# Kernel optimization log

Hardware: AMD Instinct MI355X
Metric: run time of the kernel (lower is better)

Reference implementation:

```python
import jax, jax.numpy as jnp
import numpy as np

EMBED = 384
HEADS = 12
DH = EMBED // HEADS  # 32, lucidrains default dim_heads = dim // heads
EPS = 1e-5


def _layernorm(t, g, b):
    mu = jnp.mean(t, axis=-1, keepdims=True)
    var = jnp.mean(jnp.square(t - mu), axis=-1, keepdims=True)
    return (t - mu) * jax.lax.rsqrt(var + EPS) * g + b


def _self_attn(t2, Wq, Wkv, Wo, bo):
    # t2: (N, T, D) -> multi-head self attention (lucidrains SelfAttention)
    N, T, D = t2.shape
    q = t2 @ Wq
    k, v = jnp.split(t2 @ Wkv, 2, axis=-1)
    def split_heads(z):
        return z.reshape(N, T, HEADS, DH).transpose(0, 2, 1, 3)  # (N,H,T,DH)
    q, k, v = map(split_heads, (q, k, v))
    dots = jnp.einsum('nhie,nhje->nhij', q, k) * (DH ** -0.5)
    o = jnp.einsum('nhij,nhje->nhie', jax.nn.softmax(dots, axis=-1), v)
    o = o.transpose(0, 2, 1, 3).reshape(N, T, D)
    return o @ Wo + bo


def _axial(xcl, axis, Wq, Wkv, Wo, bo):
    # xcl channels-last: (b, 3, 16, 16, C); attend along `axis` (1, 2 or 3)
    y = jnp.moveaxis(xcl, axis, -2)
    sh = y.shape
    o = _self_attn(y.reshape(-1, sh[-2], sh[-1]), Wq, Wkv, Wo, bo)
    return jnp.moveaxis(o.reshape(sh), -2, axis)


def setup_inputs() -> dict:
    key = jax.random.key(0)
    ks = jax.random.split(key, 24)
    d, mlp = EMBED, 4 * EMBED
    s = 0.02
    inp = {'x': jax.random.normal(ks[0], (128, 384, 3, 16, 16), jnp.float32)}
    for i in range(3):  # one SelfAttention per axial dim (slice, h, w)
        inp[f'Wq{i}'] = (jax.random.normal(ks[1 + 3 * i], (d, d)) * s).astype(jnp.float32)
        inp[f'Wkv{i}'] = (jax.random.normal(ks[2 + 3 * i], (d, 2 * d)) * s).astype(jnp.float32)
        inp[f'Wo{i}'] = (jax.random.normal(ks[3 + 3 * i], (d, d)) * s).astype(jnp.float32)
        inp[f'bo{i}'] = jnp.zeros((d,), jnp.float32)
    inp['g1'] = jnp.ones((d,), jnp.float32)
    inp['be1'] = jnp.zeros((d,), jnp.float32)
    inp['W1m'] = (jax.random.normal(ks[10], (d, mlp)) * s).astype(jnp.float32)
    inp['b1m'] = jnp.zeros((mlp,), jnp.float32)
    inp['W2m'] = (jax.random.normal(ks[11], (mlp, d)) * s).astype(jnp.float32)
    inp['b2m'] = jnp.zeros((d,), jnp.float32)
    inp['g2'] = jnp.ones((d,), jnp.float32)
    inp['be2'] = jnp.zeros((d,), jnp.float32)
    return inp


def reference(x, Wq0, Wkv0, Wo0, bo0, Wq1, Wkv1, Wo1, bo1, Wq2, Wkv2, Wo2, bo2,
              g1, be1, W1m, b1m, W2m, b2m, g2, be2):
    # x: (B, C=384, 3, 16, 16); dropout is identity in eval mode
    xcl = jnp.moveaxis(x, 1, -1)  # (B, 3, 16, 16, C)
    attn = (_axial(xcl, 1, Wq0, Wkv0, Wo0, bo0)
            + _axial(xcl, 2, Wq1, Wkv1, Wo1, bo1)
            + _axial(xcl, 3, Wq2, Wkv2, Wo2, bo2))  # sum_axial_out=True
    xcl = xcl + attn  # residual
    B = xcl.shape[0]
    t = xcl.reshape(B, 3 * 16 * 16, EMBED)  # == x.flatten(2).transpose(1,2)
    t = _layernorm(t, g1, be1)
    m = jax.nn.gelu(t @ W1m + b1m, approximate=False) @ W2m + b2m
    t = _layernorm(t + m, g2, be2)
    return jnp.moveaxis(t.reshape(B, 3, 16, 16, EMBED), -1, 1)
```

## Files before the change

### kernel.cpp

```cpp
#include <hip/hip_runtime.h>

typedef unsigned short u16;
typedef __bf16 bf16;
typedef bf16  bf16x4 __attribute__((ext_vector_type(4)));
typedef bf16  bf16x8 __attribute__((ext_vector_type(8)));
typedef float f32x4  __attribute__((ext_vector_type(4)));

__device__ __forceinline__ u16  f2b(float v) { return __builtin_bit_cast(u16, (bf16)v); }
__device__ __forceinline__ float b2f(u16 b)  { return (float)__builtin_bit_cast(bf16, b); }

__global__ void probe_dtype(const float* xf, int* flag) {
    __shared__ int cnt[256];
    const int tid = threadIdx.x;
    int good = 0;
#pragma unroll
    for (int i = 0; i < 4; ++i) {
        const float a = fabsf(xf[tid * 4 + i]);
        if (a > 9.5e-7f && a < 1.0e6f) good++;
    }
    cnt[tid] = good;
    __syncthreads();
    if (tid == 0) { int s = 0; for (int i = 0; i < 256; ++i) s += cnt[i]; *flag = (s > 512) ? 1 : 0; }
}

__global__ void cvt_vec(const void* in, bf16* out, int n, const int* flag) {
    const int f32 = *flag;
    for (int i = blockIdx.x * 256 + threadIdx.x; i < n; i += gridDim.x * 256)
        out[i] = f32 ? (bf16)(((const float*)in)[i])
                     : __builtin_bit_cast(bf16, ((const u16*)in)[i]);
}

__global__ void transpose_cvt(const void* in, u16* out, size_t base_off, int R, int C, const int* flag) {
    __shared__ u16 tile[32][34];
    const int f32 = *flag;
    const int c0 = blockIdx.x * 32, r0 = blockIdx.y * 32;
    const size_t bi = base_off + (size_t)blockIdx.z * R * C;
    const size_t bo = (size_t)blockIdx.z * R * C;
    const int tx = threadIdx.x, ty = threadIdx.y;
#pragma unroll
    for (int i = 0; i < 4; ++i) {
        const size_t idx = bi + (size_t)(r0 + ty + i * 8) * C + c0 + tx;
        tile[ty + i * 8][tx] = f32 ? f2b(((const float*)in)[idx]) : ((const u16*)in)[idx];
    }
    __syncthreads();
#pragma unroll
    for (int i = 0; i < 4; ++i)
        out[bo + (size_t)(c0 + ty + i * 8) * R + r0 + tx] = tile[tx][ty + i * 8];
}

__global__ void transpose_out(const u16* in, void* out, size_t base_off, int R, int C, const int* flag) {
    __shared__ u16 tile[32][34];
    const int f32 = *flag;
    const int c0 = blockIdx.x * 32, r0 = blockIdx.y * 32;
    const size_t bi = (size_t)blockIdx.z * R * C;
    const size_t bo = base_off + (size_t)blockIdx.z * R * C;
    const int tx = threadIdx.x, ty = threadIdx.y;
#pragma unroll
    for (int i = 0; i < 4; ++i)
        tile[ty + i * 8][tx] = in[bi + (size_t)(r0 + ty + i * 8) * C + c0 + tx];
    __syncthreads();
#pragma unroll
    for (int i = 0; i < 4; ++i) {
        const size_t o = bo + (size_t)(c0 + ty + i * 8) * R + r0 + tx;
        const u16 v = tile[tx][ty + i * 8];
        if (f32) ((float*)out)[o] = b2f(v); else ((u16*)out)[o] = v;
    }
}

__device__ __forceinline__ void gld_lds16(const bf16* g, bf16* l) {
    __builtin_amdgcn_global_load_lds((__attribute__((address_space(1))) void*)g,
                                     (__attribute__((address_space(3))) void*)l,
                                     16, 0, 0);
}

template<int MODE>
__global__ __launch_bounds__(256)
void gemm_bt(const bf16* __restrict__ A, const bf16* __restrict__ BT,
             bf16* C, const bf16* __restrict__ bias,
             const bf16* add, int M, int N, int K)
{
    __shared__ __align__(16) bf16 sm[4][8192];
    const int tid = threadIdx.x;

    const int gx = gridDim.x, gy = gridDim.y;
    int lin = blockIdx.y * gx + blockIdx.x;
    const int nwg = gx * gy;
    const int q = nwg >> 3, r8 = nwg & 7;
    const int xcd = lin & 7, idx = lin >> 3;
    lin = (xcd < r8 ? xcd * (q + 1) : r8 * (q + 1) + (xcd - r8) * q) + idx;
    const int bm0 = (lin / gy) * 128;
    const int bn0 = (lin % gy) * 128;

    const int lane = tid & 63, wid = tid >> 6;
    const int wr = wid >> 1, wc = wid & 1;
    const int fr = lane & 15, fg = lane >> 4;
    const int arow = tid >> 3;
    const int scol = ((tid & 7) ^ (arow & 7)) << 3;

    const bf16* Ab = A  + (size_t)(bm0 + arow) * K + scol;
    const bf16* Bb = BT + (size_t)(bn0 + arow) * K + scol;

    f32x4 acc[4][4] = {};

    const int NT = K >> 6;
    {
        bf16* la = sm[0];
        bf16* lb = sm[1];
#pragma unroll
        for (int i = 0; i < 4; ++i) gld_lds16(Ab + (size_t)i * 32 * K, &la[i * 2048 + tid * 8]);
#pragma unroll
        for (int i = 0; i < 4; ++i) gld_lds16(Bb + (size_t)i * 32 * K, &lb[i * 2048 + tid * 8]);
    }
    __syncthreads();

    const int sw = fr & 7;
    for (int t = 0; t < NT; ++t) {
        if (t + 1 < NT) {
            const int k0 = (t + 1) << 6;
            bf16* la = sm[2 * ((t + 1) & 1)];
            bf16* lb = sm[2 * ((t + 1) & 1) + 1];
#pragma unroll
            for (int i = 0; i < 4; ++i) gld_lds16(Ab + k0 + (size_t)i * 32 * K, &la[i * 2048 + tid * 8]);
#pragma unroll
            for (int i = 0; i < 4; ++i) gld_lds16(Bb + k0 + (size_t)i * 32 * K, &lb[i * 2048 + tid * 8]);
        }
        const bf16* la = sm[2 * (t & 1)];
        const bf16* lb = sm[2 * (t & 1) + 1];
#pragma unroll
        for (int kk = 0; kk < 2; ++kk) {
            bf16x8 af[4], bfv[4];
#pragma unroll
            for (int m = 0; m < 4; ++m) {
                const int rr = wr * 64 + m * 16 + fr;
                af[m] = *(const bf16x8*)&la[rr * 64 + ((((kk << 2) + fg) ^ sw) << 3)];
            }
#pragma unroll
            for (int n = 0; n < 4; ++n) {
                const int rr = wc * 64 + n * 16 + fr;
                bfv[n] = *(const bf16x8*)&lb[rr * 64 + ((((kk << 2) + fg) ^ sw) << 3)];
            }
#pragma unroll
            for (int m = 0; m < 4; ++m)
#pragma unroll
                for (int n = 0; n < 4; ++n)
                    acc[m][n] = __builtin_amdgcn_mfma_f32_16x16x32_bf16(af[m], bfv[n], acc[m][n], 0, 0, 0);
        }
        __syncthreads();
    }

    float* lc = (float*)sm;
#pragma unroll
    for (int n = 0; n < 4; ++n) {
        const int col = wc * 64 + n * 16 + fr;
#pragma unroll
        for (int m = 0; m < 4; ++m) {
            const int row0 = wr * 64 + m * 16 + fg * 4;
#pragma unroll
            for (int r2 = 0; r2 < 4; ++r2)
                lc[(row0 + r2) * 128 + col] = acc[m][n][r2];
        }
    }
    __syncthreads();
    const f32x4* lc4 = (const f32x4*)sm;
#pragma unroll
    for (int i = 0; i < 16; ++i) {
        const int chunk = i * 256 + tid;
        const int row = chunk >> 5, cb = (chunk & 31) * 4;
        const size_t goff = (size_t)(bm0 + row) * N + bn0 + cb;
        const f32x4 v = lc4[chunk];
        bf16x4 o;
        if (MODE == 0) {
#pragma unroll
            for (int e = 0; e < 4; ++e) o[e] = (bf16)v[e];
        } else if (MODE == 1) {
            const bf16x4 bv = *(const bf16x4*)&bias[bn0 + cb];
            const bf16x4 av = *(const bf16x4*)&add[goff];
#pragma unroll
            for (int e = 0; e < 4; ++e) o[e] = (bf16)(v[e] + (float)bv[e] + (float)av[e]);
        } else {
            const bf16x4 bv = *(const bf16x4*)&bias[bn0 + cb];
#pragma unroll
            for (int e = 0; e < 4; ++e) {
                const float x = v[e] + (float)bv[e];
                o[e] = (bf16)(0.5f * x * (1.f + erff(x * 0.70710678118654752f)));
            }
        }
        *(bf16x4*)&C[goff] = o;
    }
}

__global__ __launch_bounds__(256)
void attn16(const bf16* __restrict__ QKV, bf16* __restrict__ O, int tstride, int lastmul)
{
    const int lane = threadIdx.x & 63;
    const int gw   = (blockIdx.x * 256 + threadIdx.x) >> 6;
    const int head = gw % 12;
    const int seq  = gw / 12;
    const int b    = seq / 48, r2 = seq % 48;
    const int s    = r2 >> 4, last = r2 & 15;
    const int tbase = b * 768 + s * 256 + last * lastmul;
    const int fr = lane & 15, fg = lane >> 4;

    const size_t rowQ = (size_t)(tbase + fr * tstride) * 1152 + head * 32 + fg * 8;
    const bf16x8 kf = *(const bf16x8*)(QKV + rowQ + 384);
    const bf16x8 qf = *(const bf16x8*)(QKV + rowQ);
    const f32x4 z = {0.f, 0.f, 0.f, 0.f};
    f32x4 S = __builtin_amdgcn_mfma_f32_16x16x32_bf16(kf, qf, z, 0, 0, 0);

    const float sc = 0.17677669529663687f;
    float mx = fmaxf(fmaxf(S[0], S[1]), fmaxf(S[2], S[3]));
    mx = fmaxf(mx, __shfl_xor(mx, 16));
    mx = fmaxf(mx, __shfl_xor(mx, 32));
    float p[4], sum = 0.f;
#pragma unroll
    for (int r = 0; r < 4; ++r) { p[r] = __expf((S[r] - mx) * sc); sum += p[r]; }
    sum += __shfl_xor(sum, 16);
    sum += __shfl_xor(sum, 32);
    const float inv = 1.f / sum;

    bf16x8 pa;
#pragma unroll
    for (int j = 0; j < 8; ++j) {
        const int srcg = 2 * fg + (j >> 2);
        const float v = __shfl(p[j & 3], fr + 16 * (srcg & 3));
        pa[j] = (bf16)(fg < 2 ? v * inv : 0.f);
    }

#pragma unroll
    for (int t = 0; t < 2; ++t) {
        bf16x8 vf;
#pragma unroll
        for (int j = 0; j < 8; ++j) {
            const int key = fg * 8 + j;
            vf[j] = (fg < 2)
                ? QKV[(size_t)(tbase + key * tstride) * 1152 + 768 + head * 32 + fr + 16 * t]
                : (bf16)0.f;
        }
        f32x4 o = __builtin_amdgcn_mfma_f32_16x16x32_bf16(pa, vf, z, 0, 0, 0);
#pragma unroll
        for (int r = 0; r < 4; ++r)
            O[(size_t)(tbase + (fg * 4 + r) * tstride) * 384 + head * 32 + fr + 16 * t] = (bf16)o[r];
    }
}

__global__ __launch_bounds__(256)
void attn3(const bf16* __restrict__ QKV, bf16* __restrict__ O)
{
    const int t    = blockIdx.x * 256 + threadIdx.x;
    const int head = t % 12;
    const int seq  = t / 12;
    const int b    = seq >> 8, hw = seq & 255;
    const size_t base  = (size_t)(b * 768 + hw) * 1152 + head * 32;
    const size_t tstep = (size_t)256 * 1152;

    float s[3][3] = {};
#pragma unroll
    for (int c = 0; c < 4; ++c) {
        bf16x8 q[3], k[3];
#pragma unroll
        for (int i = 0; i < 3; ++i) {
            q[i] = *(const bf16x8*)(QKV + base + i * tstep + c * 8);
            k[i] = *(const bf16x8*)(QKV + base + i * tstep + 384 + c * 8);
        }
#pragma unroll
        for (int i = 0; i < 3; ++i)
#pragma unroll
            for (int j = 0; j < 3; ++j) {
                float a = 0.f;
#pragma unroll
                for (int e = 0; e < 8; ++e) a += (float)q[i][e] * (float)k[j][e];
                s[i][j] += a;
            }
    }
    const float sc = 0.17677669529663687f;
    float p[3][3];
#pragma unroll
    for (int i = 0; i < 3; ++i) {
        const float mx = fmaxf(s[i][0], fmaxf(s[i][1], s[i][2]));
        float sum = 0.f;
#pragma unroll
        for (int j = 0; j < 3; ++j) { p[i][j] = __expf((s[i][j] - mx) * sc); sum += p[i][j]; }
        const float inv = 1.f / sum;
#pragma unroll
        for (int j = 0; j < 3; ++j) p[i][j] *= inv;
    }
    const size_t obase = (size_t)(b * 768 + hw) * 384 + head * 32;
#pragma unroll
    for (int c = 0; c < 4; ++c) {
        bf16x8 v[3];
#pragma unroll
        for (int j = 0; j < 3; ++j) v[j] = *(const bf16x8*)(QKV + base + j * tstep + 768 + c * 8);
#pragma unroll
        for (int i = 0; i < 3; ++i) {
            bf16x8 ov;
#pragma unroll
            for (int e = 0; e < 8; ++e)
                ov[e] = (bf16)(p[i][0] * (float)v[0][e] + p[i][1] * (float)v[1][e] + p[i][2] * (float)v[2][e]);
            *(bf16x8*)(O + obase + (size_t)i * 256 * 384 + c * 8) = ov;
        }
    }
}

__global__ __launch_bounds__(256)
void ln_kernel(const bf16* __restrict__ in, bf16* __restrict__ out,
               const bf16* __restrict__ g, const bf16* __restrict__ be, int ntok)
{
    const int w    = (blockIdx.x * 256 + threadIdx.x) >> 6;
    const int lane = threadIdx.x & 63;
    if (w >= ntok) return;
    const bf16* row = in + (size_t)w * 384;
    float x[6], sum = 0.f;
#pragma unroll
    for (int i = 0; i < 6; ++i) { x[i] = (float)row[lane + i * 64]; sum += x[i]; }
#pragma unroll
    for (int o = 32; o >= 1; o >>= 1) sum += __shfl_xor(sum, o);
    const float mu = sum * (1.f / 384.f);
    float vs = 0.f;
#pragma unroll
    for (int i = 0; i < 6; ++i) { const float d = x[i] - mu; vs += d * d; }
#pragma unroll
    for (int o = 32; o >= 1; o >>= 1) vs += __shfl_xor(vs, o);
    const float rstd = rsqrtf(vs * (1.f / 384.f) + 1e-5f);
    bf16* orow = out + (size_t)w * 384;
#pragma unroll
    for (int i = 0; i < 6; ++i)
        orow[lane + i * 64] = (bf16)((x[i] - mu) * rstd * (float)g[lane + i * 64] + (float)be[lane + i * 64]);
}

extern "C" void kernel_launch(void* const* d_in, const int* in_sizes, int n_in,
                              void* d_out, int out_size, void* d_ws, size_t ws_size,
                              hipStream_t stream)
{
    const void* x = d_in[0];
    const void *Wq[3], *Wkv[3], *Wo[3], *bo[3];
    for (int i = 0; i < 3; ++i) {
        Wq[i]  = d_in[1 + 4 * i];
        Wkv[i] = d_in[2 + 4 * i];
        Wo[i]  = d_in[3 + 4 * i];
        bo[i]  = d_in[4 + 4 * i];
    }
    const void* g1  = d_in[13];
    const void* be1 = d_in[14];
    const void* W1m = d_in[15];
    const void* b1m = d_in[16];
    const void* W2m = d_in[17];
    const void* b2m = d_in[18];
    const void* g2  = d_in[19];
    const void* be2 = d_in[20];

    char* ws = (char*)d_ws;
    const size_t WB = 6ull * 1024 * 1024;
    bf16* wqkvT[3]; bf16* woT[3];
    for (int i = 0; i < 3; ++i) {
        wqkvT[i] = (bf16*)(ws + (size_t)i * 884736ull);
        woT[i]   = (bf16*)(ws + 2654208ull + (size_t)i * 294912ull);
    }
    bf16* w1mT = (bf16*)(ws + 3538944ull);
    bf16* w2mT = (bf16*)(ws + 4718592ull);
    bf16* vbo[3]; bf16 *vg1, *vbe1, *vg2, *vbe2, *vb1m, *vb2m;
    {
        char* vp = ws + 5898240ull;
        vbo[0] = (bf16*)(vp);            vbo[1] = (bf16*)(vp + 768);  vbo[2] = (bf16*)(vp + 1536);
        vg1  = (bf16*)(vp + 2304);       vbe1 = (bf16*)(vp + 3072);
        vg2  = (bf16*)(vp + 3840);       vbe2 = (bf16*)(vp + 4608);
        vb1m = (bf16*)(vp + 5376);       vb2m = (bf16*)(vp + 8448);
    }
    int* dflag = (int*)(ws + 5908480ull);

    int NB = 32;
    while (NB > 1) {
        size_t need = WB + (size_t)NB * 768 * (4 * 384 + 1536) * 2;
        if (need <= ws_size) break;
        NB >>= 1;
    }
    const int Tc = NB * 768;
    const size_t tokB = (size_t)Tc * 384 * 2;
    bf16* Xc   = (bf16*)(ws + WB);
    bf16* ABc  = (bf16*)(ws + WB + tokB);
    bf16* T1c  = (bf16*)(ws + WB + 2 * tokB);
    bf16* ATOc = (bf16*)(ws + WB + 3 * tokB);
    bf16* BIGc = (bf16*)(ws + WB + 4 * tokB);

    probe_dtype<<<1, 256, 0, stream>>>((const float*)x, dflag);
    for (int i = 0; i < 3; ++i)
        cvt_vec<<<2, 256, 0, stream>>>(bo[i], vbo[i], 384, dflag);
    cvt_vec<<<2, 256, 0, stream>>>(g1,  vg1,  384,  dflag);
    cvt_vec<<<2, 256, 0, stream>>>(be1, vbe1, 384,  dflag);
    cvt_vec<<<2, 256, 0, stream>>>(g2,  vg2,  384,  dflag);
    cvt_vec<<<2, 256, 0, stream>>>(be2, vbe2, 384,  dflag);
    cvt_vec<<<6, 256, 0, stream>>>(b1m, vb1m, 1536, dflag);
    cvt_vec<<<2, 256, 0, stream>>>(b2m, vb2m, 384,  dflag);

    const dim3 tb(32, 8);
    for (int i = 0; i < 3; ++i) {
        transpose_cvt<<<dim3(12, 12, 1), tb, 0, stream>>>(Wq[i],  (u16*)wqkvT[i],               0, 384, 384, dflag);
        transpose_cvt<<<dim3(24, 12, 1), tb, 0, stream>>>(Wkv[i], (u16*)(wqkvT[i] + 384 * 384), 0, 384, 768, dflag);
        transpose_cvt<<<dim3(12, 12, 1), tb, 0, stream>>>(Wo[i],  (u16*)woT[i],                 0, 384, 384, dflag);
    }
    transpose_cvt<<<dim3(48, 12, 1), tb, 0, stream>>>(W1m, (u16*)w1mT, 0, 384, 1536, dflag);
    transpose_cvt<<<dim3(12, 48, 1), tb, 0, stream>>>(W2m, (u16*)w2mT, 0, 1536, 384, dflag);

    for (int b0 = 0; b0 < 128; b0 += NB) {
        const size_t xoff = (size_t)b0 * 384 * 768;
        transpose_cvt<<<dim3(24, 12, NB), tb, 0, stream>>>(x, (u16*)Xc, xoff, 384, 768, dflag);

        for (int i = 0; i < 3; ++i) {
            gemm_bt<0><<<dim3(Tc / 128, 9), 256, 0, stream>>>(Xc, wqkvT[i], BIGc, nullptr, nullptr, Tc, 1152, 384);
            if (i == 0)      attn3 <<<NB * 12,  256, 0, stream>>>(BIGc, ATOc);
            else if (i == 1) attn16<<<NB * 144, 256, 0, stream>>>(BIGc, ATOc, 16, 1);
            else             attn16<<<NB * 144, 256, 0, stream>>>(BIGc, ATOc, 1, 16);
            gemm_bt<1><<<dim3(Tc / 128, 3), 256, 0, stream>>>(ATOc, woT[i], ABc, vbo[i], (i == 0) ? Xc : ABc, Tc, 384, 384);
        }
        ln_kernel<<<Tc / 4, 256, 0, stream>>>(ABc, T1c, vg1, vbe1, Tc);
        gemm_bt<2><<<dim3(Tc / 128, 12), 256, 0, stream>>>(T1c, w1mT, BIGc, vb1m, nullptr, Tc, 1536, 384);
        gemm_bt<1><<<dim3(Tc / 128, 3),  256, 0, stream>>>(BIGc, w2mT, ABc, vb2m, T1c, Tc, 384, 1536);
        ln_kernel<<<Tc / 4, 256, 0, stream>>>(ABc, Xc, vg2, vbe2, Tc);
        transpose_out<<<dim3(12, 24, NB), tb, 0, stream>>>((const u16*)Xc, d_out, xoff, 768, 384, dflag);
    }
}
```

Measured before the change: 1.559 ms.

## Fuse three axial QKV projections into one 256-tile GEMM, add 256-tile MLP up GEMM

Concatenates the three per-axis QKV weight matrices into one 3584-row weight, zero-padded from 3456 rows. A new 256x256-tile, 512-thread GEMM computes all Q/K/V projections in a single launch, and the attention kernels read from it with a wider row stride. The same larger-tile kernel also replaces the MLP up-projection with fused GELU, and it writes bf16 through LDS with vector stores. The intent is fewer launches, more reuse of the A tile, and better MFMA efficiency. The cost is a larger intermediate buffer, which can lower the chunk size NB, plus 128 padded rows of wasted compute and 128 KB of LDS per block.

```diff
diff --git a/kernel.cpp b/kernel.cpp
--- a/kernel.cpp
+++ b/kernel.cpp
@@ -28,6 +28,10 @@
     for (int i = blockIdx.x * 256 + threadIdx.x; i < n; i += gridDim.x * 256)
         out[i] = f32 ? (bf16)(((const float*)in)[i])
                      : __builtin_bit_cast(bf16, ((const u16*)in)[i]);
+}
+
+__global__ void zfill(bf16* p, int n) {
+    for (int i = blockIdx.x * 256 + threadIdx.x; i < n; i += gridDim.x * 256) p[i] = (bf16)0.f;
 }
 
 __global__ void transpose_cvt(const void* in, u16* out, size_t base_off, int R, int C, const int* flag) {
@@ -71,6 +75,101 @@
     __builtin_amdgcn_global_load_lds((__attribute__((address_space(1))) void*)g,
                                      (__attribute__((address_space(3))) void*)l,
                                      16, 0, 0);
+}
+
+template<int MODE>
+__global__ __launch_bounds__(512)
+void gemm256(const bf16* __restrict__ A, const bf16* __restrict__ BT,
+             bf16* C, const bf16* __restrict__ bias, int M, int N, int K)
+{
+    __shared__ __align__(16) bf16 sm[65536];
+    const int tid = threadIdx.x;
+
+    const int gx = gridDim.x, gy = gridDim.y;
+    int lin = blockIdx.y * gx + blockIdx.x;
+    const int nwg = gx * gy;
+    const int q = nwg >> 3, r8 = nwg & 7;
+    const int xcd = lin & 7, idx = lin >> 3;
+    lin = (xcd < r8 ? xcd * (q + 1) : r8 * (q + 1) + (xcd - r8) * q) + idx;
+    const int bm0 = (lin / gy) * 256;
+    const int bn0 = (lin % gy) * 256;
+
+    const int lane = tid & 63, wid = tid >> 6;
+    const int wr = wid >> 2, wc = wid & 3;
+    const int fr = lane & 15, fg = lane >> 4;
+    const int arow = tid >> 3;
+    const int scol = ((tid & 7) ^ (arow & 7)) << 3;
+
+    const bf16* Ab = A  + (size_t)(bm0 + arow) * K + scol;
+    const bf16* Bb = BT + (size_t)(bn0 + arow) * K + scol;
+
+    bf16* const lA0 = sm;
+    bf16* const lA1 = sm + 16384;
+    bf16* const lB0 = sm + 32768;
+    bf16* const lB1 = sm + 49152;
+
+    f32x4 acc[8][4] = {};
+    const int NT = K >> 6;
+
+#pragma unroll
+    for (int i = 0; i < 4; ++i) gld_lds16(Ab + (size_t)i * 64 * K, lA0 + i * 4096 + tid * 8);
+#pragma unroll
+    for (int i = 0; i < 4; ++i) gld_lds16(Bb + (size_t)i * 64 * K, lB0 + i * 4096 + tid * 8);
+    __syncthreads();
+
+    const int sw = fr & 7;
+    for (int t = 0; t < NT; ++t) {
+        if (t + 1 < NT) {
+            const int k0 = (t + 1) << 6;
+            bf16* la = ((t + 1) & 1) ? lA1 : lA0;
+            bf16* lb = ((t + 1) & 1) ? lB1 : lB0;
+#pragma unroll
+            for (int i = 0; i < 4; ++i) gld_lds16(Ab + k0 + (size_t)i * 64 * K, la + i * 4096 + tid * 8);
+#pragma unroll
+            for (int i = 0; i < 4; ++i) gld_lds16(Bb + k0 + (size_t)i * 64 * K, lb + i * 4096 + tid * 8);
+        }
+        const bf16* la = (t & 1) ? lA1 : lA0;
+        const bf16* lb = (t & 1) ? lB1 : lB0;
+#pragma unroll
+        for (int kk = 0; kk < 2; ++kk) {
+            const int so = ((((kk << 2) + fg) ^ sw) << 3);
+            bf16x8 bfv[4];
+#pragma unroll
+            for (int n = 0; n < 4; ++n)
+                bfv[n] = *(const bf16x8*)&lb[(wc * 64 + n * 16 + fr) * 64 + so];
+#pragma unroll
+            for (int m = 0; m < 8; ++m) {
+                const bf16x8 af = *(const bf16x8*)&la[(wr * 128 + m * 16 + fr) * 64 + so];
+#pragma unroll
+                for (int n = 0; n < 4; ++n)
+                    acc[m][n] = __builtin_amdgcn_mfma_f32_16x16x32_bf16(af, bfv[n], acc[m][n], 0, 0, 0);
+            }
+        }
+        __syncthreads();
+    }
+
+#pragma unroll
+    for (int n = 0; n < 4; ++n) {
+        const int col = wc * 64 + n * 16 + fr;
+        const float bv = (MODE == 2) ? (float)bias[bn0 + col] : 0.f;
+#pragma unroll
+        for (int m = 0; m < 8; ++m) {
+            const int row0 = wr * 128 + m * 16 + fg * 4;
+#pragma unroll
+            for (int r = 0; r < 4; ++r) {
+                float v = acc[m][n][r];
+                if (MODE == 2) { v += bv; v = 0.5f * v * (1.f + erff(v * 0.70710678118654752f)); }
+                sm[(row0 + r) * 256 + col] = (bf16)v;
+            }
+        }
+    }
+    __syncthreads();
+#pragma unroll
+    for (int it = 0; it < 16; ++it) {
+        const int chunk = it * 512 + tid;
+        const int row = chunk >> 5, c8 = (chunk & 31) << 3;
+        *(bf16x8*)&C[(size_t)(bm0 + row) * N + bn0 + c8] = *(const bf16x8*)&sm[row * 256 + c8];
+    }
 }
 
 template<int MODE>
@@ -101,7 +200,6 @@
     const bf16* Bb = BT + (size_t)(bn0 + arow) * K + scol;
 
     f32x4 acc[4][4] = {};
-
     const int NT = K >> 6;
     {
         bf16* la = sm[0];
@@ -130,15 +228,11 @@
         for (int kk = 0; kk < 2; ++kk) {
             bf16x8 af[4], bfv[4];
 #pragma unroll
-            for (int m = 0; m < 4; ++m) {
-                const int rr = wr * 64 + m * 16 + fr;
-                af[m] = *(const bf16x8*)&la[rr * 64 + ((((kk << 2) + fg) ^ sw) << 3)];
-            }
-#pragma unroll
-            for (int n = 0; n < 4; ++n) {
-                const int rr = wc * 64 + n * 16 + fr;
-                bfv[n] = *(const bf16x8*)&lb[rr * 64 + ((((kk << 2) + fg) ^ sw) << 3)];
-            }
+            for (int m = 0; m < 4; ++m)
+                af[m] = *(const bf16x8*)&la[(wr * 64 + m * 16 + fr) * 64 + ((((kk << 2) + fg) ^ sw) << 3)];
+#pragma unroll
+            for (int n = 0; n < 4; ++n)
+                bfv[n] = *(const bf16x8*)&lb[(wc * 64 + n * 16 + fr) * 64 + ((((kk << 2) + fg) ^ sw) << 3)];
 #pragma unroll
             for (int m = 0; m < 4; ++m)
 #pragma unroll
@@ -169,28 +263,21 @@
         const size_t goff = (size_t)(bm0 + row) * N + bn0 + cb;
         const f32x4 v = lc4[chunk];
         bf16x4 o;
-        if (MODE == 0) {
-#pragma unroll
-            for (int e = 0; e < 4; ++e) o[e] = (bf16)v[e];
-        } else if (MODE == 1) {
+        if (MODE == 1) {
             const bf16x4 bv = *(const bf16x4*)&bias[bn0 + cb];
             const bf16x4 av = *(const bf16x4*)&add[goff];
 #pragma unroll
             for (int e = 0; e < 4; ++e) o[e] = (bf16)(v[e] + (float)bv[e] + (float)av[e]);
         } else {
-            const bf16x4 bv = *(const bf16x4*)&bias[bn0 + cb];
-#pragma unroll
-            for (int e = 0; e < 4; ++e) {
-                const float x = v[e] + (float)bv[e];
-                o[e] = (bf16)(0.5f * x * (1.f + erff(x * 0.70710678118654752f)));
-            }
+#pragma unroll
+            for (int e = 0; e < 4; ++e) o[e] = (bf16)v[e];
         }
         *(bf16x4*)&C[goff] = o;
     }
 }
 
 __global__ __launch_bounds__(256)
-void attn16(const bf16* __restrict__ QKV, bf16* __restrict__ O, int tstride, int lastmul)
+void attn16(const bf16* __restrict__ QKV, bf16* __restrict__ O, int tstride, int lastmul, int qs)
 {
     const int lane = threadIdx.x & 63;
     const int gw   = (blockIdx.x * 256 + threadIdx.x) >> 6;
@@ -201,7 +288,7 @@
     const int tbase = b * 768 + s * 256 + last * lastmul;
     const int fr = lane & 15, fg = lane >> 4;
 
-    const size_t rowQ = (size_t)(tbase + fr * tstride) * 1152 + head * 32 + fg * 8;
+    const size_t rowQ = (size_t)(tbase + fr * tstride) * qs + head * 32 + fg * 8;
     const bf16x8 kf = *(const bf16x8*)(QKV + rowQ + 384);
     const bf16x8 qf = *(const bf16x8*)(QKV + rowQ);
     const f32x4 z = {0.f, 0.f, 0.f, 0.f};
@@ -233,7 +320,7 @@
         for (int j = 0; j < 8; ++j) {
             const int key = fg * 8 + j;
             vf[j] = (fg < 2)
-                ? QKV[(size_t)(tbase + key * tstride) * 1152 + 768 + head * 32 + fr + 16 * t]
+                ? QKV[(size_t)(tbase + key * tstride) * qs + 768 + head * 32 + fr + 16 * t]
                 : (bf16)0.f;
         }
         f32x4 o = __builtin_amdgcn_mfma_f32_16x16x32_bf16(pa, vf, z, 0, 0, 0);
@@ -244,14 +331,14 @@
 }
 
 __global__ __launch_bounds__(256)
-void attn3(const bf16* __restrict__ QKV, bf16* __restrict__ O)
+void attn3(const bf16* __restrict__ QKV, bf16* __restrict__ O, int qs)
 {
     const int t    = blockIdx.x * 256 + threadIdx.x;
     const int head = t % 12;
     const int seq  = t / 12;
     const int b    = seq >> 8, hw = seq & 255;
-    const size_t base  = (size_t)(b * 768 + hw) * 1152 + head * 32;
-    const size_t tstep = (size_t)256 * 1152;
+    const size_t base  = (size_t)(b * 768 + hw) * qs + head * 32;
+    const size_t tstep = (size_t)256 * qs;
 
     float s[3][3] = {};
 #pragma unroll
@@ -349,27 +436,25 @@
     const void* be2 = d_in[20];
 
     char* ws = (char*)d_ws;
-    const size_t WB = 6ull * 1024 * 1024;
-    bf16* wqkvT[3]; bf16* woT[3];
-    for (int i = 0; i < 3; ++i) {
-        wqkvT[i] = (bf16*)(ws + (size_t)i * 884736ull);
-        woT[i]   = (bf16*)(ws + 2654208ull + (size_t)i * 294912ull);
-    }
-    bf16* w1mT = (bf16*)(ws + 3538944ull);
-    bf16* w2mT = (bf16*)(ws + 4718592ull);
+    bf16* qkvT  = (bf16*)(ws);
+    bf16* woT[3];
+    for (int i = 0; i < 3; ++i) woT[i] = (bf16*)(ws + 2752512ull + (size_t)i * 294912ull);
+    bf16* w1mT = (bf16*)(ws + 3637248ull);
+    bf16* w2mT = (bf16*)(ws + 4816896ull);
     bf16* vbo[3]; bf16 *vg1, *vbe1, *vg2, *vbe2, *vb1m, *vb2m;
     {
-        char* vp = ws + 5898240ull;
+        char* vp = ws + 5996544ull;
         vbo[0] = (bf16*)(vp);            vbo[1] = (bf16*)(vp + 768);  vbo[2] = (bf16*)(vp + 1536);
         vg1  = (bf16*)(vp + 2304);       vbe1 = (bf16*)(vp + 3072);
         vg2  = (bf16*)(vp + 3840);       vbe2 = (bf16*)(vp + 4608);
         vb1m = (bf16*)(vp + 5376);       vb2m = (bf16*)(vp + 8448);
     }
-    int* dflag = (int*)(ws + 5908480ull);
+    int* dflag = (int*)(ws + 6006784ull);
+    const size_t WB = 6553600ull;
 
     int NB = 32;
     while (NB > 1) {
-        size_t need = WB + (size_t)NB * 768 * (4 * 384 + 1536) * 2;
+        size_t need = WB + (size_t)NB * 768 * (4 * 384 + 3584) * 2;
         if (need <= ws_size) break;
         NB >>= 1;
     }
@@ -390,12 +475,13 @@
     cvt_vec<<<2, 256, 0, stream>>>(be2, vbe2, 384,  dflag);
     cvt_vec<<<6, 256, 0, stream>>>(b1m, vb1m, 1536, dflag);
     cvt_vec<<<2, 256, 0, stream>>>(b2m, vb2m, 384,  dflag);
+    zfill<<<48, 256, 0, stream>>>(qkvT + 3456 * 384, 128 * 384);
 
     const dim3 tb(32, 8);
     for (int i = 0; i < 3; ++i) {
-        transpose_cvt<<<dim3(12, 12, 1), tb, 0, stream>>>(Wq[i],  (u16*)wqkvT[i],               0, 384, 384, dflag);
-        transpose_cvt<<<dim3(24, 12, 1), tb, 0, stream>>>(Wkv[i], (u16*)(wqkvT[i] + 384 * 384), 0, 384, 768, dflag);
-        transpose_cvt<<<dim3(12, 12, 1), tb, 0, stream>>>(Wo[i],  (u16*)woT[i],                 0, 384, 384, dflag);
+        transpose_cvt<<<dim3(12, 12, 1), tb, 0, stream>>>(Wq[i],  (u16*)(qkvT + (size_t)(i * 1152) * 384),        0, 384, 384, dflag);
+        transpose_cvt<<<dim3(24, 12, 1), tb, 0, stream>>>(Wkv[i], (u16*)(qkvT + (size_t)(i * 1152 + 384) * 384),  0, 384, 768, dflag);
+        transpose_cvt<<<dim3(12, 12, 1), tb, 0, stream>>>(Wo[i],  (u16*)woT[i],                                    0, 384, 384, dflag);
     }
     transpose_cvt<<<dim3(48, 12, 1), tb, 0, stream>>>(W1m, (u16*)w1mT, 0, 384, 1536, dflag);
     transpose_cvt<<<dim3(12, 48, 1), tb, 0, stream>>>(W2m, (u16*)w2mT, 0, 1536, 384, dflag);
@@ -404,16 +490,18 @@
         const size_t xoff = (size_t)b0 * 384 * 768;
         transpose_cvt<<<dim3(24, 12, NB), tb, 0, stream>>>(x, (u16*)Xc, xoff, 384, 768, dflag);
 
+        gemm256<0><<<dim3(Tc / 256, 14), 512, 0, stream>>>(Xc, qkvT, BIGc, nullptr, Tc, 3584, 384);
+
         for (int i = 0; i < 3; ++i) {
-            gemm_bt<0><<<dim3(Tc / 128, 9), 256, 0, stream>>>(Xc, wqkvT[i], BIGc, nullptr, nullptr, Tc, 1152, 384);
-            if (i == 0)      attn3 <<<NB * 12,  256, 0, stream>>>(BIGc, ATOc);
-            else if (i == 1) attn16<<<NB * 144, 256, 0, stream>>>(BIGc, ATOc, 16, 1);
-            else             attn16<<<NB * 144, 256, 0, stream>>>(BIGc, ATOc, 1, 16);
+            const bf16* qkv_i = BIGc + (size_t)i * 1152;
+            if (i == 0)      attn3 <<<NB * 12,  256, 0, stream>>>(qkv_i, ATOc, 3584);
+            else if (i == 1) attn16<<<NB * 144, 256, 0, stream>>>(qkv_i, ATOc, 16, 1, 3584);
+            else             attn16<<<NB * 144, 256, 0, stream>>>(qkv_i, ATOc, 1, 16, 3584);
             gemm_bt<1><<<dim3(Tc / 128, 3), 256, 0, stream>>>(ATOc, woT[i], ABc, vbo[i], (i == 0) ? Xc : ABc, Tc, 384, 384);
         }
         ln_kernel<<<Tc / 4, 256, 0, stream>>>(ABc, T1c, vg1, vbe1, Tc);
-        gemm_bt<2><<<dim3(Tc / 128, 12), 256, 0, stream>>>(T1c, w1mT, BIGc, vb1m, nullptr, Tc, 1536, 384);
-        gemm_bt<1><<<dim3(Tc / 128, 3),  256, 0, stream>>>(BIGc, w2mT, ABc, vb2m, T1c, Tc, 384, 1536);
+        gemm256<2><<<dim3(Tc / 256, 6), 512, 0, stream>>>(T1c, w1mT, BIGc, vb1m, Tc, 1536, 384);
+        gemm_bt<1><<<dim3(Tc / 128, 3), 256, 0, stream>>>(BIGc, w2mT, ABc, vb2m, T1c, Tc, 384, 1536);
         ln_kernel<<<Tc / 4, 256, 0, stream>>>(ABc, Xc, vg2, vbe2, Tc);
         transpose_out<<<dim3(12, 24, NB), tb, 0, stream>>>((const u16*)Xc, d_out, xoff, 768, 384, dflag);
     }
```

After: 1.674 ms. 1.07x slower.
